# Optimization experiments

Hardware: AMD Instinct MI355X
Metric: run time of the kernel (lower is better)

The kernel has to match this reference:

```python
import jax, jax.numpy as jnp
import numpy as np

L, B, N, D, H = 2, 4, 2048, 1024, 16
DH = D // H
HID = 4 * D
EPS = 1e-5


def setup_inputs() -> dict:
    key = jax.random.key(0)
    ks = jax.random.split(key, 8)
    s = 0.02
    return {
        "tokens": jax.random.normal(ks[0], (B, N, D), jnp.float32),
        "ln1_g": jnp.ones((L, D), jnp.float32),
        "ln1_b": jnp.zeros((L, D), jnp.float32),
        "qkv_w": jax.random.normal(ks[1], (L, 3 * D, D), jnp.float32) * s,
        "qkv_b": jnp.zeros((L, 3 * D), jnp.float32),
        "out_w": jax.random.normal(ks[2], (L, D, D), jnp.float32) * s,
        "out_b": jnp.zeros((L, D), jnp.float32),
        "ln2_g": jnp.ones((L, D), jnp.float32),
        "ln2_b": jnp.zeros((L, D), jnp.float32),
        "fc1_w": jax.random.normal(ks[3], (L, HID, D), jnp.float32) * s,
        "fc1_b": jnp.zeros((L, HID), jnp.float32),
        "fc2_w": jax.random.normal(ks[4], (L, D, HID), jnp.float32) * s,
        "fc2_b": jnp.zeros((L, D), jnp.float32),
    }


def _layernorm(x, g, b):
    mu = jnp.mean(x, axis=-1, keepdims=True)
    var = jnp.mean(jnp.square(x - mu), axis=-1, keepdims=True)
    return (x - mu) * jax.lax.rsqrt(var + EPS) * g + b


def _mha(x, qkv_w, qkv_b, out_w, out_b):
    # nn.MultiheadAttention self-attention, batch_first=True
    qkv = x @ qkv_w.T + qkv_b                        # [B,N,3D]
    q, k, v = jnp.split(qkv, 3, axis=-1)
    q = q.reshape(B, N, H, DH)
    k = k.reshape(B, N, H, DH)
    v = v.reshape(B, N, H, DH)
    scores = jnp.einsum("bqhd,bkhd->bhqk", q, k) / np.sqrt(DH).astype(np.float32)
    attn = jax.nn.softmax(scores, axis=-1)
    o = jnp.einsum("bhqk,bkhd->bqhd", attn, v).reshape(B, N, D)
    return o @ out_w.T + out_b


def reference(tokens, ln1_g, ln1_b, qkv_w, qkv_b, out_w, out_b,
              ln2_g, ln2_b, fc1_w, fc1_b, fc2_w, fc2_b):
    x = tokens
    for i in range(L):
        # NOTE: the original reassigns tokens = norm1(tokens) before residual,
        # so the residual is taken on the NORMED tokens (faithful to source).
        x = _layernorm(x, ln1_g[i], ln1_b[i])
        x = x + _mha(x, qkv_w[i], qkv_b[i], out_w[i], out_b[i])
        x = _layernorm(x, ln2_g[i], ln2_b[i])
        h = jax.nn.gelu(x @ fc1_w[i].T + fc1_b[i], approximate=False)
        x = x + (h @ fc2_w[i].T + fc2_b[i])
    return x  # proj_out / norm_out are Identity since out_dim == dim
```

## Files before the change

### kernel.cpp

```cpp
#include <hip/hip_runtime.h>
#include <cstdint>
#include <cstddef>

typedef unsigned short u16;
typedef __attribute__((ext_vector_type(8))) short bf16x8;
typedef __attribute__((ext_vector_type(8))) u16  u16x8;
typedef __attribute__((ext_vector_type(4))) u16  u16x4;
typedef __attribute__((ext_vector_type(4))) float f32x4;
typedef __attribute__((ext_vector_type(16))) float f32x16;
typedef __attribute__((ext_vector_type(4))) unsigned u32x4;

static __device__ __forceinline__ u16 f2bf(float f) {
  unsigned u = __builtin_bit_cast(unsigned, f);
  u += 0x7fffu + ((u >> 16) & 1u);
  return (u16)(u >> 16);
}
static __device__ __forceinline__ float bf2f(u16 h) {
  return __builtin_bit_cast(float, (unsigned)h << 16);
}
static __device__ __forceinline__ unsigned cvtpk_bf16(float a, float b) {
  unsigned r;
  asm("v_cvt_pk_bf16_f32 %0, %1, %2" : "=v"(r) : "v"(a), "v"(b));
  return r;
}
static __device__ __forceinline__ float rawexp2(float x) {
  float r;
  asm("v_exp_f32 %0, %1" : "=v"(r) : "v"(x));
  return r;
}

static __device__ __forceinline__ void gload16(u16* lds, const u16* g) {
  __builtin_amdgcn_global_load_lds(
      (__attribute__((address_space(1))) unsigned int*)(void*)(g),
      (__attribute__((address_space(3))) unsigned int*)(lds), 16, 0, 0);
}

__global__ __launch_bounds__(256) void cast_f32_bf16(
    const float* __restrict__ s, u16* __restrict__ d, int n4) {
  int i = blockIdx.x * 256 + threadIdx.x;
  if (i < n4) {
    float4 v = ((const float4*)s)[i];
    u16x4 o;
    o[0] = f2bf(v.x); o[1] = f2bf(v.y); o[2] = f2bf(v.z); o[3] = f2bf(v.w);
    ((u16x4*)d)[i] = o;
  }
}

__global__ __launch_bounds__(256) void ln_kernel(
    const float* __restrict__ in, const float* __restrict__ g,
    const float* __restrict__ bb, float* __restrict__ outf,
    u16* __restrict__ outb) {
  const int row = blockIdx.x;
  const int t = threadIdx.x;
  const float4 v = ((const float4*)(in + (size_t)row * 1024))[t];
  float s  = v.x + v.y + v.z + v.w;
  float sq = v.x * v.x + v.y * v.y + v.z * v.z + v.w * v.w;
#pragma unroll
  for (int off = 32; off > 0; off >>= 1) {
    s  += __shfl_down(s, off);
    sq += __shfl_down(sq, off);
  }
  __shared__ float red[8];
  const int w = t >> 6;
  if ((t & 63) == 0) { red[w] = s; red[4 + w] = sq; }
  __syncthreads();
  const float ts  = red[0] + red[1] + red[2] + red[3];
  const float tsq = red[4] + red[5] + red[6] + red[7];
  const float mu = ts * (1.0f / 1024.0f);
  const float rv = rsqrtf(tsq * (1.0f / 1024.0f) - mu * mu + 1e-5f);
  const float4 gv = ((const float4*)g)[t];
  const float4 bv = ((const float4*)bb)[t];
  float4 y;
  y.x = (v.x - mu) * rv * gv.x + bv.x;
  y.y = (v.y - mu) * rv * gv.y + bv.y;
  y.z = (v.z - mu) * rv * gv.z + bv.z;
  y.w = (v.w - mu) * rv * gv.w + bv.w;
  ((float4*)(outf + (size_t)row * 1024))[t] = y;
  u16x4 ob;
  ob[0] = f2bf(y.x); ob[1] = f2bf(y.y); ob[2] = f2bf(y.z); ob[3] = f2bf(y.w);
  *(u16x4*)(outb + (size_t)row * 1024 + t * 4) = ob;
}

#define BM 128
#define BN 128
#define BK 64

template <int MODE>
__global__ __launch_bounds__(256) void gemm_bt(
    const u16* __restrict__ A, const u16* __restrict__ W,
    const float* __restrict__ bias, const float* __restrict__ res,
    u16* __restrict__ outb, float* __restrict__ outf, int Nn, int K) {
  __shared__ u16 As[BM * BK];
  __shared__ u16 Bs[BN * BK];
  const int t  = threadIdx.x;
  const int w  = t >> 6;
  const int ln = t & 63;
  const int lr = ln & 15;
  const int lg = ln >> 4;
  const int bm = blockIdx.x * BM;
  const int bn = blockIdx.y * BN;
  const int wm = (w >> 1) * 64;
  const int wn = (w & 1) * 64;

  f32x4 acc[4][4] = {};

  const int srow = t >> 3;
  const int scol = 8 * ((t & 7) ^ (srow & 7));
  const u16* gA = A + (size_t)(bm + srow) * K + scol;
  const u16* gB = W + (size_t)(bn + srow) * K + scol;
  const char* const AsB = (const char*)As;
  const char* const BsB = (const char*)Bs;

  const int kSteps = K >> 6;
  for (int kt = 0; kt < kSteps; ++kt) {
    __syncthreads();
    const u16* ga = gA + kt * BK;
    const u16* gb = gB + kt * BK;
#pragma unroll
    for (int c = 0; c < 4; ++c) {
      gload16(As + c * 2048 + w * 512, ga + (size_t)(c * 32) * K);
      gload16(Bs + c * 2048 + w * 512, gb + (size_t)(c * 32) * K);
    }
    __syncthreads();

#pragma unroll
    for (int kc = 0; kc < 2; ++kc) {
      bf16x8 af[4], bfr[4];
#pragma unroll
      for (int mi = 0; mi < 4; ++mi) {
        const int row = wm + mi * 16 + lr;
        af[mi] = *(const bf16x8*)(
            AsB + ((row * 128 + kc * 64 + lg * 16) ^ ((row & 7) << 4)));
      }
#pragma unroll
      for (int ni = 0; ni < 4; ++ni) {
        const int row = wn + ni * 16 + lr;
        bfr[ni] = *(const bf16x8*)(
            BsB + ((row * 128 + kc * 64 + lg * 16) ^ ((row & 7) << 4)));
      }
#pragma unroll
      for (int mi = 0; mi < 4; ++mi)
#pragma unroll
        for (int ni = 0; ni < 4; ++ni)
          acc[mi][ni] = __builtin_amdgcn_mfma_f32_16x16x32_bf16(
              af[mi], bfr[ni], acc[mi][ni], 0, 0, 0);
    }
  }

#pragma unroll
  for (int ni = 0; ni < 4; ++ni) {
    const int col = bn + wn + ni * 16 + lr;
    const float bv = bias[col];
#pragma unroll
    for (int mi = 0; mi < 4; ++mi) {
      const int row0 = bm + wm + mi * 16 + lg * 4;
#pragma unroll
      for (int r = 0; r < 4; ++r) {
        float v = acc[mi][ni][r] + bv;
        const size_t idx = (size_t)(row0 + r) * Nn + col;
        if (MODE == 1) v = 0.5f * v * (1.0f + erff(v * 0.70710678118654752f));
        if (MODE == 2) outf[idx] = res[idx] + v;
        else           outb[idx] = f2bf(v);
      }
    }
  }
}

__global__ __launch_bounds__(256)
__attribute__((amdgpu_waves_per_eu(4, 4))) void attn_kernel(
    const u16* __restrict__ qkv, u16* __restrict__ o) {
  __shared__ u16 Ks[2 * 64 * 64];
  __shared__ u16 Vt[2 * 64 * 64];
  const int t   = threadIdx.x;
  const int w   = t >> 6;
  const int l   = t & 63;
  const int q31 = l & 31;
  const int h   = l >> 5;
  const int Lid = blockIdx.x;
  const int v_id = (Lid & 7) * 128 + (Lid >> 3);
  const int bh = v_id >> 4;
  const int b  = bh >> 4;
  const int hd = bh & 15;
  const int qb = (v_id & 15) * 128;
  const size_t baseRow = (size_t)b * 2048;
  const int hcol = hd * 64;
  const float FIXMAX = 16.0f;

  bf16x8 qf[4];
  {
    const u16* qp = qkv + (baseRow + qb + w * 32 + q31) * 3072 + hcol + h * 8;
    const float qscale = 0.125f * 1.44269504088896f;
#pragma unroll
    for (int f = 0; f < 4; ++f) {
      u16x8 raw = *(const u16x8*)(qp + f * 16);
      bf16x8 q;
#pragma unroll
      for (int i = 0; i < 8; ++i)
        q[i] = (short)f2bf(bf2f(raw[i]) * qscale);
      qf[f] = q;
    }
  }

  f32x16 oacc[2] = {};
  float lrun = 0.0f;

  const int skey = t >> 3;
  const int dK   = 8 * ((t & 7) ^ (skey & 7));
  const int sd0  = (t & 7) * 8;

  {
    gload16(Ks + w * 512,        qkv + (baseRow + skey) * 3072      + 1024 + hcol + dK);
    gload16(Ks + 2048 + w * 512, qkv + (baseRow + 32 + skey) * 3072 + 1024 + hcol + dK);
    u16x8 va = *(const u16x8*)(qkv + (baseRow + skey) * 3072      + 2048 + hcol + sd0);
    u16x8 vb = *(const u16x8*)(qkv + (baseRow + 32 + skey) * 3072 + 2048 + hcol + sd0);
    char* VtB = (char*)Vt;
#pragma unroll
    for (int j = 0; j < 8; ++j) {
      const int sw = (j ^ (t & 7)) << 4;
      *(u16*)(VtB + ((((sd0 + j) * 128 + skey * 2)        ) ^ sw)) = va[j];
      *(u16*)(VtB + ((((sd0 + j) * 128 + (32 + skey) * 2) ) ^ sw)) = vb[j];
    }
  }
  __syncthreads();

  for (int kt = 0; kt < 32; ++kt) {
    char* const KsB = (char*)Ks + (kt & 1) * 8192;
    char* const VtB = (char*)Vt + (kt & 1) * 8192;
    u16* const KsN  = Ks + ((kt & 1) ^ 1) * 4096;
    char* const VtN = (char*)Vt + ((kt & 1) ^ 1) * 8192;

    u16x8 vva, vvb;
    const bool pf = (kt < 31);
    if (pf) {
      const size_t krow = baseRow + (size_t)(kt + 1) * 64;
      gload16(KsN + w * 512,        qkv + (krow + skey) * 3072      + 1024 + hcol + dK);
      gload16(KsN + 2048 + w * 512, qkv + (krow + 32 + skey) * 3072 + 1024 + hcol + dK);
      vva = *(const u16x8*)(qkv + (krow + skey) * 3072      + 2048 + hcol + sd0);
      vvb = *(const u16x8*)(qkv + (krow + 32 + skey) * 3072 + 2048 + hcol + sd0);
    }

    f32x16 s0 = {}, s1 = {};
#pragma unroll
    for (int f = 0; f < 4; ++f) {
      const int d0b = (f * 16 + h * 8) * 2;
      {
        const int row = q31;
        bf16x8 ka = *(const bf16x8*)(KsB + ((row * 128 + d0b) ^ ((row & 7) << 4)));
        s0 = __builtin_amdgcn_mfma_f32_32x32x16_bf16(ka, qf[f], s0, 0, 0, 0);
      }
      {
        const int row = 32 + q31;
        bf16x8 ka = *(const bf16x8*)(KsB + ((row * 128 + d0b) ^ ((row & 7) << 4)));
        s1 = __builtin_amdgcn_mfma_f32_32x32x16_bf16(ka, qf[f], s1, 0, 0, 0);
      }
    }

#pragma unroll
    for (int r = 0; r < 16; ++r) {
      s0[r] = rawexp2(s0[r] - FIXMAX);
      s1[r] = rawexp2(s1[r] - FIXMAX);
    }
    float tsum[16];
#pragma unroll
    for (int r = 0; r < 16; ++r) tsum[r] = s0[r] + s1[r];
#pragma unroll
    for (int st = 8; st >= 1; st >>= 1)
#pragma unroll
      for (int r = 0; r < st; ++r) tsum[r] += tsum[r + st];
    lrun += tsum[0] + __shfl_xor(tsum[0], 32);

#pragma unroll
    for (int kw = 0; kw < 4; ++kw) {
      const int w1 = kw & 1;
      const f32x16 sv = (kw < 2) ? s0 : s1;
      const unsigned L0 = cvtpk_bf16(sv[8 * w1 + 0], sv[8 * w1 + 1]);
      const unsigned L1 = cvtpk_bf16(sv[8 * w1 + 2], sv[8 * w1 + 3]);
      const unsigned H0 = cvtpk_bf16(sv[8 * w1 + 4], sv[8 * w1 + 5]);
      const unsigned H1 = cvtpk_bf16(sv[8 * w1 + 6], sv[8 * w1 + 7]);
      const unsigned X0 = h ? L0 : H0;
      const unsigned X1 = h ? L1 : H1;
      const unsigned R0 = (unsigned)__shfl_xor((int)X0, 32);
      const unsigned R1 = (unsigned)__shfl_xor((int)X1, 32);
      u32x4 pw;
      pw[0] = h ? R0 : L0;
      pw[1] = h ? R1 : L1;
      pw[2] = h ? H0 : R0;
      pw[3] = h ? H1 : R1;
      const bf16x8 pb = __builtin_bit_cast(bf16x8, pw);
      const int k0b = (kw * 16 + h * 8) * 2;
#pragma unroll
      for (int dt = 0; dt < 2; ++dt) {
        const int d = dt * 32 + q31;
        bf16x8 va = *(const bf16x8*)(
            VtB + ((d * 128 + k0b) ^ ((((d & 7) ^ ((d >> 3) & 7))) << 4)));
        oacc[dt] = __builtin_amdgcn_mfma_f32_32x32x16_bf16(va, pb, oacc[dt], 0, 0, 0);
      }
    }

    if (pf) {
#pragma unroll
      for (int j = 0; j < 8; ++j) {
        const int sw = (j ^ (t & 7)) << 4;
        *(u16*)(VtN + ((((sd0 + j) * 128 + skey * 2)        ) ^ sw)) = vva[j];
        *(u16*)(VtN + ((((sd0 + j) * 128 + (32 + skey) * 2) ) ^ sw)) = vvb[j];
      }
    }
    __syncthreads();
  }

  const float inv = 1.0f / lrun;
  const size_t orow = baseRow + qb + w * 32 + q31;
#pragma unroll
  for (int dt = 0; dt < 2; ++dt)
#pragma unroll
    for (int g = 0; g < 4; ++g) {
      u16x4 ov;
#pragma unroll
      for (int j = 0; j < 4; ++j) ov[j] = f2bf(oacc[dt][g * 4 + j] * inv);
      *(u16x4*)(o + orow * 1024 + hcol + dt * 32 + g * 8 + h * 4) = ov;
    }
}

extern "C" void kernel_launch(void* const* d_in, const int* in_sizes, int n_in,
                              void* d_out, int out_size, void* d_ws,
                              size_t ws_size, hipStream_t stream) {
  const float* tokens = (const float*)d_in[0];
  const float* ln1_g  = (const float*)d_in[1];
  const float* ln1_b  = (const float*)d_in[2];
  const float* qkv_w  = (const float*)d_in[3];
  const float* qkv_b  = (const float*)d_in[4];
  const float* out_w  = (const float*)d_in[5];
  const float* out_b  = (const float*)d_in[6];
  const float* ln2_g  = (const float*)d_in[7];
  const float* ln2_b  = (const float*)d_in[8];
  const float* fc1_w  = (const float*)d_in[9];
  const float* fc1_b  = (const float*)d_in[10];
  const float* fc2_w  = (const float*)d_in[11];
  const float* fc2_b  = (const float*)d_in[12];
  float* xf = (float*)d_out;

  char* ws = (char*)d_ws;
  size_t off = 0;
  auto take = [&](size_t bytes) {
    char* p = ws + off;
    off += (bytes + 255) & ~(size_t)255;
    return p;
  };
  u16* xn    = (u16*)take((size_t)8192 * 1024 * 2);
  u16* big   = (u16*)take((size_t)8192 * 4096 * 2);
  u16* attnb = (u16*)take((size_t)8192 * 1024 * 2);
  u16* qkvw  = (u16*)take((size_t)2 * 3072 * 1024 * 2);
  u16* outw  = (u16*)take((size_t)2 * 1024 * 1024 * 2);
  u16* fc1w  = (u16*)take((size_t)2 * 4096 * 1024 * 2);
  u16* fc2w  = (u16*)take((size_t)2 * 1024 * 4096 * 2);
  u16* qkvb16 = big;
  u16* hb     = big;

  cast_f32_bf16<<<6144, 256, 0, stream>>>(qkv_w, qkvw, 2 * 3072 * 1024 / 4);
  cast_f32_bf16<<<2048, 256, 0, stream>>>(out_w, outw, 2 * 1024 * 1024 / 4);
  cast_f32_bf16<<<8192, 256, 0, stream>>>(fc1_w, fc1w, 2 * 4096 * 1024 / 4);
  cast_f32_bf16<<<8192, 256, 0, stream>>>(fc2_w, fc2w, 2 * 1024 * 4096 / 4);

  for (int i = 0; i < 2; ++i) {
    ln_kernel<<<8192, 256, 0, stream>>>(i == 0 ? tokens : xf,
                                        ln1_g + i * 1024, ln1_b + i * 1024, xf, xn);
    gemm_bt<0><<<dim3(64, 24), 256, 0, stream>>>(
        xn, qkvw + (size_t)i * 3072 * 1024, qkv_b + i * 3072, nullptr,
        qkvb16, nullptr, 3072, 1024);
    attn_kernel<<<1024, 256, 0, stream>>>(qkvb16, attnb);
    gemm_bt<2><<<dim3(64, 8), 256, 0, stream>>>(
        attnb, outw + (size_t)i * 1024 * 1024, out_b + i * 1024, xf,
        nullptr, xf, 1024, 1024);
    ln_kernel<<<8192, 256, 0, stream>>>(xf, ln2_g + i * 1024, ln2_b + i * 1024,
                                        xf, xn);
    gemm_bt<1><<<dim3(64, 32), 256, 0, stream>>>(
        xn, fc1w + (size_t)i * 4096 * 1024, fc1_b + i * 4096, nullptr,
        hb, nullptr, 4096, 1024);
    gemm_bt<2><<<dim3(64, 8), 256, 0, stream>>>(
        hb, fc2w + (size_t)i * 1024 * 4096, fc2_b + i * 1024, xf,
        nullptr, xf, 1024, 4096);
  }
}
```

Baseline: 900.7 us.

## Split-K the N=1024 GEMMs and fold partial-sum reduction into layernorm

The out-projection and fc2 GEMMs, which had only 512 tiles, now run as split-K with two K halves writing fp32 partials to a workspace. The partials, bias and residual are summed inside a fused layernorm kernel, with a final reduce kernel after the last layer. This doubles the block count so the GPU is better occupied on the narrow GEMMs. In exchange it writes and reads two extra fp32 activation buffers (about 64 MB of traffic per GEMM).

```diff
diff --git a/kernel.cpp b/kernel.cpp
--- a/kernel.cpp
+++ b/kernel.cpp
@@ -9,6 +9,8 @@
 typedef __attribute__((ext_vector_type(4))) float f32x4;
 typedef __attribute__((ext_vector_type(16))) float f32x16;
 typedef __attribute__((ext_vector_type(4))) unsigned u32x4;
+
+#define MROW ((size_t)8192 * 1024)
 
 static __device__ __forceinline__ u16 f2bf(float f) {
   unsigned u = __builtin_bit_cast(unsigned, f);
@@ -81,6 +83,68 @@
   *(u16x4*)(outb + (size_t)row * 1024 + t * 4) = ob;
 }
 
+__global__ __launch_bounds__(256) void ln_fused(
+    const float* __restrict__ in, const float* __restrict__ p0,
+    const float* __restrict__ p1, const float* __restrict__ gbias,
+    const float* __restrict__ g, const float* __restrict__ bb,
+    float* __restrict__ outf, u16* __restrict__ outb) {
+  const int row = blockIdx.x;
+  const int t = threadIdx.x;
+  const size_t ro = (size_t)row * 1024;
+  float4 v  = ((const float4*)(in + ro))[t];
+  const float4 a0 = ((const float4*)(p0 + ro))[t];
+  const float4 a1 = ((const float4*)(p1 + ro))[t];
+  const float4 bi = ((const float4*)gbias)[t];
+  v.x += a0.x + a1.x + bi.x;
+  v.y += a0.y + a1.y + bi.y;
+  v.z += a0.z + a1.z + bi.z;
+  v.w += a0.w + a1.w + bi.w;
+  float s  = v.x + v.y + v.z + v.w;
+  float sq = v.x * v.x + v.y * v.y + v.z * v.z + v.w * v.w;
+#pragma unroll
+  for (int off = 32; off > 0; off >>= 1) {
+    s  += __shfl_down(s, off);
+    sq += __shfl_down(sq, off);
+  }
+  __shared__ float red[8];
+  const int w = t >> 6;
+  if ((t & 63) == 0) { red[w] = s; red[4 + w] = sq; }
+  __syncthreads();
+  const float ts  = red[0] + red[1] + red[2] + red[3];
+  const float tsq = red[4] + red[5] + red[6] + red[7];
+  const float mu = ts * (1.0f / 1024.0f);
+  const float rv = rsqrtf(tsq * (1.0f / 1024.0f) - mu * mu + 1e-5f);
+  const float4 gv = ((const float4*)g)[t];
+  const float4 bv = ((const float4*)bb)[t];
+  float4 y;
+  y.x = (v.x - mu) * rv * gv.x + bv.x;
+  y.y = (v.y - mu) * rv * gv.y + bv.y;
+  y.z = (v.z - mu) * rv * gv.z + bv.z;
+  y.w = (v.w - mu) * rv * gv.w + bv.w;
+  ((float4*)(outf + ro))[t] = y;
+  u16x4 ob;
+  ob[0] = f2bf(y.x); ob[1] = f2bf(y.y); ob[2] = f2bf(y.z); ob[3] = f2bf(y.w);
+  *(u16x4*)(outb + ro + t * 4) = ob;
+}
+
+__global__ __launch_bounds__(256) void reduce_out(
+    const float* __restrict__ in, const float* __restrict__ p0,
+    const float* __restrict__ p1, const float* __restrict__ gbias,
+    float* __restrict__ outf) {
+  const int row = blockIdx.x;
+  const int t = threadIdx.x;
+  const size_t ro = (size_t)row * 1024;
+  float4 v  = ((const float4*)(in + ro))[t];
+  const float4 a0 = ((const float4*)(p0 + ro))[t];
+  const float4 a1 = ((const float4*)(p1 + ro))[t];
+  const float4 bi = ((const float4*)gbias)[t];
+  v.x += a0.x + a1.x + bi.x;
+  v.y += a0.y + a1.y + bi.y;
+  v.z += a0.z + a1.z + bi.z;
+  v.w += a0.w + a1.w + bi.w;
+  ((float4*)(outf + ro))[t] = v;
+}
+
 #define BM 128
 #define BN 128
 #define BK 64
@@ -89,7 +153,8 @@
 __global__ __launch_bounds__(256) void gemm_bt(
     const u16* __restrict__ A, const u16* __restrict__ W,
     const float* __restrict__ bias, const float* __restrict__ res,
-    u16* __restrict__ outb, float* __restrict__ outf, int Nn, int K) {
+    u16* __restrict__ outb, float* __restrict__ outf, int Nn, int K,
+    int Kstride) {
   __shared__ u16 As[BM * BK];
   __shared__ u16 Bs[BN * BK];
   const int t  = threadIdx.x;
@@ -101,13 +166,14 @@
   const int bn = blockIdx.y * BN;
   const int wm = (w >> 1) * 64;
   const int wn = (w & 1) * 64;
+  const int kz = (MODE == 3) ? (int)blockIdx.z * K : 0;
 
   f32x4 acc[4][4] = {};
 
   const int srow = t >> 3;
   const int scol = 8 * ((t & 7) ^ (srow & 7));
-  const u16* gA = A + (size_t)(bm + srow) * K + scol;
-  const u16* gB = W + (size_t)(bn + srow) * K + scol;
+  const u16* gA = A + (size_t)(bm + srow) * Kstride + kz + scol;
+  const u16* gB = W + (size_t)(bn + srow) * Kstride + kz + scol;
   const char* const AsB = (const char*)As;
   const char* const BsB = (const char*)Bs;
 
@@ -118,8 +184,8 @@
     const u16* gb = gB + kt * BK;
 #pragma unroll
     for (int c = 0; c < 4; ++c) {
-      gload16(As + c * 2048 + w * 512, ga + (size_t)(c * 32) * K);
-      gload16(Bs + c * 2048 + w * 512, gb + (size_t)(c * 32) * K);
+      gload16(As + c * 2048 + w * 512, ga + (size_t)(c * 32) * Kstride);
+      gload16(Bs + c * 2048 + w * 512, gb + (size_t)(c * 32) * Kstride);
     }
     __syncthreads();
 
@@ -147,10 +213,12 @@
     }
   }
 
+  float* const outp = (MODE == 3) ? outf + (size_t)blockIdx.z * MROW : outf;
+
 #pragma unroll
   for (int ni = 0; ni < 4; ++ni) {
     const int col = bn + wn + ni * 16 + lr;
-    const float bv = bias[col];
+    const float bv = (MODE == 3) ? 0.0f : bias[col];
 #pragma unroll
     for (int mi = 0; mi < 4; ++mi) {
       const int row0 = bm + wm + mi * 16 + lg * 4;
@@ -159,8 +227,9 @@
         float v = acc[mi][ni][r] + bv;
         const size_t idx = (size_t)(row0 + r) * Nn + col;
         if (MODE == 1) v = 0.5f * v * (1.0f + erff(v * 0.70710678118654752f));
-        if (MODE == 2) outf[idx] = res[idx] + v;
-        else           outb[idx] = f2bf(v);
+        if (MODE == 2)      outf[idx] = res[idx] + v;
+        else if (MODE == 3) outp[idx] = v;
+        else                outb[idx] = f2bf(v);
       }
     }
   }
@@ -349,12 +418,15 @@
   u16* xn    = (u16*)take((size_t)8192 * 1024 * 2);
   u16* big   = (u16*)take((size_t)8192 * 4096 * 2);
   u16* attnb = (u16*)take((size_t)8192 * 1024 * 2);
+  float* part = (float*)take(2 * MROW * 4);
   u16* qkvw  = (u16*)take((size_t)2 * 3072 * 1024 * 2);
   u16* outw  = (u16*)take((size_t)2 * 1024 * 1024 * 2);
   u16* fc1w  = (u16*)take((size_t)2 * 4096 * 1024 * 2);
   u16* fc2w  = (u16*)take((size_t)2 * 1024 * 4096 * 2);
   u16* qkvb16 = big;
   u16* hb     = big;
+  float* p0 = part;
+  float* p1 = part + MROW;
 
   cast_f32_bf16<<<6144, 256, 0, stream>>>(qkv_w, qkvw, 2 * 3072 * 1024 / 4);
   cast_f32_bf16<<<2048, 256, 0, stream>>>(out_w, outw, 2 * 1024 * 1024 / 4);
@@ -362,22 +434,28 @@
   cast_f32_bf16<<<8192, 256, 0, stream>>>(fc2_w, fc2w, 2 * 1024 * 4096 / 4);
 
   for (int i = 0; i < 2; ++i) {
-    ln_kernel<<<8192, 256, 0, stream>>>(i == 0 ? tokens : xf,
-                                        ln1_g + i * 1024, ln1_b + i * 1024, xf, xn);
+    if (i == 0)
+      ln_kernel<<<8192, 256, 0, stream>>>(tokens, ln1_g, ln1_b, xf, xn);
+    else
+      ln_fused<<<8192, 256, 0, stream>>>(xf, p0, p1, fc2_b + (i - 1) * 1024,
+                                         ln1_g + i * 1024, ln1_b + i * 1024,
+                                         xf, xn);
     gemm_bt<0><<<dim3(64, 24), 256, 0, stream>>>(
         xn, qkvw + (size_t)i * 3072 * 1024, qkv_b + i * 3072, nullptr,
-        qkvb16, nullptr, 3072, 1024);
+        qkvb16, nullptr, 3072, 1024, 1024);
     attn_kernel<<<1024, 256, 0, stream>>>(qkvb16, attnb);
-    gemm_bt<2><<<dim3(64, 8), 256, 0, stream>>>(
-        attnb, outw + (size_t)i * 1024 * 1024, out_b + i * 1024, xf,
-        nullptr, xf, 1024, 1024);
-    ln_kernel<<<8192, 256, 0, stream>>>(xf, ln2_g + i * 1024, ln2_b + i * 1024,
-                                        xf, xn);
+    gemm_bt<3><<<dim3(64, 8, 2), 256, 0, stream>>>(
+        attnb, outw + (size_t)i * 1024 * 1024, nullptr, nullptr,
+        nullptr, part, 1024, 512, 1024);
+    ln_fused<<<8192, 256, 0, stream>>>(xf, p0, p1, out_b + i * 1024,
+                                       ln2_g + i * 1024, ln2_b + i * 1024,
+                                       xf, xn);
     gemm_bt<1><<<dim3(64, 32), 256, 0, stream>>>(
         xn, fc1w + (size_t)i * 4096 * 1024, fc1_b + i * 4096, nullptr,
-        hb, nullptr, 4096, 1024);
-    gemm_bt<2><<<dim3(64, 8), 256, 0, stream>>>(
-        hb, fc2w + (size_t)i * 1024 * 4096, fc2_b + i * 1024, xf,
-        nullptr, xf, 1024, 4096);
-  }
-}
+        hb, nullptr, 4096, 1024, 1024);
+    gemm_bt<3><<<dim3(64, 8, 2), 256, 0, stream>>>(
+        hb, fc2w + (size_t)i * 1024 * 4096, nullptr, nullptr,
+        nullptr, part, 1024, 2048, 4096);
+  }
+  reduce_out<<<8192, 256, 0, stream>>>(xf, p0, p1, fc2_b + 1024, xf);
+}
```

Result: slower. 1.014 ms (+12.6%).
